# Kernel tuning notes

Hardware: AMD Instinct MI355X
Metric: run time of the kernel (lower is better)

Reference implementation:

```python
import jax, jax.numpy as jnp
import numpy as np

B, T, C, H = 2, 2048, 1024, 16
R = 32
LORA_SCALE = 0.5  # lora_alpha / r = (0.5*rank) / rank
HD = C // H


def setup_inputs() -> dict:
    key = jax.random.key(0)
    ks = jax.random.split(key, 8)
    std = 0.02
    return {
        "x": jax.random.normal(ks[0], (B, T, C), jnp.float32),
        "w_attn": jax.random.normal(ks[1], (3 * C, C), jnp.float32) * std,
        "b_attn": jnp.zeros((3 * C,), jnp.float32),
        "la_attn": jax.random.normal(ks[2], (R, C), jnp.float32) * std,
        "lb_attn": jax.random.normal(ks[3], (3 * C, R), jnp.float32) * std,
        "w_proj": jax.random.normal(ks[4], (C, C), jnp.float32) * std,
        "b_proj": jnp.zeros((C,), jnp.float32),
        "la_proj": jax.random.normal(ks[5], (R, C), jnp.float32) * std,
        "lb_proj": jax.random.normal(ks[6], (C, R), jnp.float32) * std,
    }


def lora_linear(x, w, b, la, lb):
    # y = x @ W^T + b + scale * (x @ A^T) @ B^T
    return x @ w.T + b + LORA_SCALE * ((x @ la.T) @ lb.T)


def reference(x, w_attn, b_attn, la_attn, lb_attn, w_proj, b_proj, la_proj, lb_proj):
    Bsz, Tlen, Cdim = x.shape
    qkv = lora_linear(x, w_attn, b_attn, la_attn, lb_attn)  # [B,T,3C]
    q, k, v = jnp.split(qkv, 3, axis=2)
    # [B,T,C] -> [B,H,T,hd]
    rs = lambda t: t.reshape(Bsz, Tlen, H, HD).transpose(0, 2, 1, 3)
    q, k, v = rs(q), rs(k), rs(v)
    att = jnp.einsum("bhqd,bhkd->bhqk", q, k) * (1.0 / np.sqrt(HD))
    causal = jnp.tril(jnp.ones((Tlen, Tlen), dtype=bool))
    att = jnp.where(causal[None, None], att, -jnp.inf)
    att = jax.nn.softmax(att, axis=-1)
    y = jnp.einsum("bhqk,bhkd->bhqd", att, v)  # [B,H,T,hd]
    y = y.transpose(0, 2, 1, 3).reshape(Bsz, Tlen, Cdim)
    return lora_linear(y, w_proj, b_proj, la_proj, lb_proj)
```

## Files before the change

kernel.cpp:

```cpp
#include <hip/hip_runtime.h>
#include <hip/hip_bf16.h>


typedef __attribute__((ext_vector_type(8))) short short8;
typedef __attribute__((ext_vector_type(4))) float float4v;

#define QSCALE 0.18033688011112292f

static __device__ __forceinline__ float b2f(ushort u) {
  union { uint i; float f; } v; v.i = ((uint)u) << 16; return v.f;
}
static __device__ __forceinline__ ushort f2b(float f) {
  union { float f; uint i; } v; v.f = f;
  uint i = v.i + 0x7fffu + ((v.i >> 16) & 1u);
  return (ushort)(i >> 16);
}
static __device__ __forceinline__ float4v zero4() {
  float4v z = {0.f, 0.f, 0.f, 0.f}; return z;
}
static __device__ __forceinline__ void glld16(const void* g, void* l) {
  __builtin_amdgcn_global_load_lds((const __attribute__((address_space(1))) void*)g,
                                   (__attribute__((address_space(3))) void*)l,
                                   16, 0, 0);
}

__global__ __launch_bounds__(256) void convert_all(
    const float* __restrict__ x, const float* __restrict__ wa,
    const float* __restrict__ la, const float* __restrict__ lb,
    const float* __restrict__ wp, const float* __restrict__ lp,
    const float* __restrict__ lq,
    ushort* __restrict__ xb, ushort* __restrict__ wab, ushort* __restrict__ lab,
    ushort* __restrict__ lbb, ushort* __restrict__ wpb, ushort* __restrict__ lpb,
    ushort* __restrict__ lqb) {
  const int stride = gridDim.x * blockDim.x;
  for (int i = blockIdx.x * blockDim.x + threadIdx.x; i < 2146304; i += stride) {
    const float* s; ushort* d; int off;
    if (i < 1048576)      { s = x;  d = xb;  off = i; }
    else if (i < 1835008) { s = wa; d = wab; off = i - 1048576; }
    else if (i < 1843200) { s = la; d = lab; off = i - 1835008; }
    else if (i < 1867776) { s = lb; d = lbb; off = i - 1843200; }
    else if (i < 2129920) { s = wp; d = wpb; off = i - 1867776; }
    else if (i < 2138112) { s = lp; d = lpb; off = i - 2129920; }
    else                  { s = lq; d = lqb; off = i - 2138112; }
    float4 v = ((const float4*)s)[off];
    union { ushort u[4]; uint2 p; } o;
    o.u[0] = f2b(v.x); o.u[1] = f2b(v.y); o.u[2] = f2b(v.z); o.u[3] = f2b(v.w);
    ((uint2*)d)[off] = o.p;
  }
}

__global__ __launch_bounds__(256) void lora_t(
    const ushort* __restrict__ X, const ushort* __restrict__ La,
    ushort* __restrict__ T) {
  const int tid = threadIdx.x;
  const int m = blockIdx.x * 8 + (tid >> 5);
  const int r = tid & 31;
  const uint4* xr = (const uint4*)(X + (size_t)m * 1024);
  const uint4* lr = (const uint4*)(La + (size_t)r * 1024);
  float s = 0.f;
#pragma unroll 4
  for (int kk = 0; kk < 128; ++kk) {
    uint4 xv = xr[kk], lv = lr[kk];
    s += b2f((ushort)xv.x) * b2f((ushort)lv.x) + b2f((ushort)(xv.x >> 16)) * b2f((ushort)(lv.x >> 16));
    s += b2f((ushort)xv.y) * b2f((ushort)lv.y) + b2f((ushort)(xv.y >> 16)) * b2f((ushort)(lv.y >> 16));
    s += b2f((ushort)xv.z) * b2f((ushort)lv.z) + b2f((ushort)(xv.z >> 16)) * b2f((ushort)(lv.z >> 16));
    s += b2f((ushort)xv.w) * b2f((ushort)lv.w) + b2f((ushort)(xv.w >> 16)) * b2f((ushort)(lv.w >> 16));
  }
  T[(size_t)m * 32 + r] = f2b(0.5f * s);
}

template <bool OUTF32, bool VSPLIT, int NBX>
__global__ __launch_bounds__(256) void gemm_lora(
    const ushort* __restrict__ A, const ushort* __restrict__ W,
    const float* __restrict__ bias,
    const ushort* __restrict__ T1, const ushort* __restrict__ Lb,
    void* __restrict__ outv, ushort* __restrict__ vt, int K, int ldo) {
  __shared__ __attribute__((aligned(16))) ushort As[2][128 * 32];
  __shared__ __attribute__((aligned(16))) ushort Ws[2][128 * 32];
  const int tid = threadIdx.x;
  const int lane = tid & 63, wv = tid >> 6;
  const int l15 = lane & 15, quad = lane >> 4;
  const int L = blockIdx.x;
  const int x8 = L & 7, q = L >> 3;
  const int bx = q % NBX;
  const int by = x8 * 4 + q / NBX;
  const int m0 = by * 128, n0 = bx * 128;
  const int wm = (wv >> 1) * 64, wn = (wv & 1) * 64;
  const int r4 = lane >> 2, c4 = (lane & 3) * 8;
  const int KT = K >> 5;

  float4v acc[4][4];
#pragma unroll
  for (int i = 0; i < 4; i++)
#pragma unroll
    for (int j = 0; j < 4; j++) acc[i][j] = zero4();

  auto stage = [&](int t, int buf) {
    const ushort* sA; const ushort* sW; int ld, k0;
    if (t < KT) { sA = A; sW = W; ld = K; k0 = t * 32; }
    else        { sA = T1; sW = Lb; ld = 32; k0 = 0; }
#pragma unroll
    for (int u = 0; u < 2; ++u) {
      int R = wv * 32 + u * 16;
      glld16(sA + (size_t)(m0 + R + r4) * ld + k0 + c4, &As[buf][R * 32]);
      glld16(sW + (size_t)(n0 + R + r4) * ld + k0 + c4, &Ws[buf][R * 32]);
    }
  };

  stage(0, 0);
  for (int t = 0; t <= KT; ++t) {
    __syncthreads();
    if (t < KT) stage(t + 1, (t + 1) & 1);
    const int b = t & 1;
    short8 af[4], wf[4];
#pragma unroll
    for (int i = 0; i < 4; i++)
      af[i] = *(const short8*)&As[b][(wm + i * 16 + l15) * 32 + quad * 8];
#pragma unroll
    for (int j = 0; j < 4; j++)
      wf[j] = *(const short8*)&Ws[b][(wn + j * 16 + l15) * 32 + quad * 8];
#pragma unroll
    for (int i = 0; i < 4; i++)
#pragma unroll
      for (int j = 0; j < 4; j++)
        acc[i][j] = __builtin_amdgcn_mfma_f32_16x16x32_bf16(af[i], wf[j], acc[i][j], 0, 0, 0);
  }

  const float qsc = (VSPLIT && n0 < 1024) ? QSCALE : 1.0f;
#pragma unroll
  for (int i = 0; i < 4; i++) {
    int gm = m0 + wm + i * 16 + quad * 4;
#pragma unroll
    for (int j = 0; j < 4; j++) {
      int gn = n0 + wn + j * 16 + l15;
      float bb = bias[gn];
      if (VSPLIT && n0 >= 2048) {
        int vc = gn - 2048;
        int bb2 = gm >> 11, t = gm & 2047;
        ushort u0 = f2b(acc[i][j][0] + bb), u1 = f2b(acc[i][j][1] + bb);
        ushort u2 = f2b(acc[i][j][2] + bb), u3 = f2b(acc[i][j][3] + bb);
        uint2 pk; pk.x = (uint)u0 | ((uint)u1 << 16); pk.y = (uint)u2 | ((uint)u3 << 16);
        *(uint2*)(vt + ((size_t)bb2 * 1024 + vc) * 2048 + t) = pk;
      } else {
#pragma unroll
        for (int r = 0; r < 4; r++) {
          float val = (acc[i][j][r] + bb) * qsc;
          if (OUTF32) ((float*)outv)[(size_t)(gm + r) * ldo + gn] = val;
          else        ((ushort*)outv)[(size_t)(gm + r) * ldo + gn] = f2b(val);
        }
      }
    }
  }
}

__global__ __launch_bounds__(256) void flash_attn(
    const ushort* __restrict__ qk, const ushort* __restrict__ vt,
    ushort* __restrict__ y) {
  __shared__ __attribute__((aligned(16))) ushort Ks[2][64 * 64];
  __shared__ __attribute__((aligned(16))) ushort Vts[2][64 * 64];
  __shared__ __attribute__((aligned(16))) ushort Ps[4 * 32 * 68];
  const int tid = threadIdx.x;
  const int lane = tid & 63, wv = tid >> 6;
  const int l15 = lane & 15, quad = lane >> 4;
  const int bid = blockIdx.x;
  const int idx = bid & 255;
  const int bh = idx & 31;
  const int g = idx >> 5;
  const int qb = (bid < 256) ? (15 - g) : g;
  const int b = bh >> 4, h = bh & 15;
  const ushort* qbase = qk + (size_t)b * 2048 * 2048 + h * 64;
  const ushort* kbase = qk + (size_t)b * 2048 * 2048 + 1024 + h * 64;
  const ushort* vbase = vt + ((size_t)b * 1024 + h * 64) * 2048;
  const int r8 = lane >> 3, c8 = (lane & 7) * 8;
  const int rotc = (c8 + r8 * 8) & 63;
  const int colk0 = (quad * 8 + 64 - 8 * (l15 & 7)) & 63;
  const int colk1 = (colk0 + 32) & 63;

#pragma unroll
  for (int u = 0; u < 4; ++u) {
    int R = wv * 32 + u * 8;
    glld16(qbase + (size_t)(qb * 128 + R + r8) * 2048 + rotc, &Ps[R * 64]);
  }
#pragma unroll
  for (int u = 0; u < 2; ++u) {
    int R = wv * 16 + u * 8;
    glld16(kbase + (size_t)(R + r8) * 2048 + rotc, &Ks[0][R * 64]);
    glld16(vbase + (size_t)(R + r8) * 2048 + rotc, &Vts[0][R * 64]);
  }
  __syncthreads();
  short8 aq[2][2];
#pragma unroll
  for (int i = 0; i < 2; ++i) {
    const int w = wv * 32 + i * 16 + l15;
    aq[i][0] = *(const short8*)&Ps[w * 64 + colk0];
    aq[i][1] = *(const short8*)&Ps[w * 64 + colk1];
  }
  __syncthreads();

  short8 ones;
#pragma unroll
  for (int e = 0; e < 8; e++) ones[e] = (short)0x3F80;

  float4v acc[2][4];
  float4v lacc[2];
#pragma unroll
  for (int i = 0; i < 2; ++i) {
    lacc[i] = zero4();
#pragma unroll
    for (int jt = 0; jt < 4; jt++) acc[i][jt] = zero4();
  }
  const int last = 2 * qb + 1;
  const int pB = wv * 32 * 68;

  for (int kb = 0; kb <= last; ++kb) {
    const int cur = kb & 1;
    if (kb < last) {
      const int nb = cur ^ 1;
#pragma unroll
      for (int u = 0; u < 2; ++u) {
        int R = wv * 16 + u * 8;
        glld16(kbase + (size_t)((kb + 1) * 64 + R + r8) * 2048 + rotc, &Ks[nb][R * 64]);
        glld16(vbase + (size_t)(R + r8) * 2048 + (kb + 1) * 64 + rotc, &Vts[nb][R * 64]);
      }
    }
    float4v s[2][4];
#pragma unroll
    for (int i = 0; i < 2; ++i)
#pragma unroll
      for (int j = 0; j < 4; ++j) s[i][j] = zero4();
#pragma unroll
    for (int j = 0; j < 4; ++j) {
      short8 bk0 = *(const short8*)&Ks[cur][(j * 16 + l15) * 64 + colk0];
      short8 bk1 = *(const short8*)&Ks[cur][(j * 16 + l15) * 64 + colk1];
#pragma unroll
      for (int i = 0; i < 2; ++i) {
        s[i][j] = __builtin_amdgcn_mfma_f32_16x16x32_bf16(aq[i][0], bk0, s[i][j], 0, 0, 0);
        s[i][j] = __builtin_amdgcn_mfma_f32_16x16x32_bf16(aq[i][1], bk1, s[i][j], 0, 0, 0);
      }
    }
#pragma unroll
    for (int i = 0; i < 2; ++i) {
      const int qrow_i = qb * 128 + wv * 32 + i * 16;
      if (kb * 64 + 63 > qrow_i) {
#pragma unroll
        for (int j = 0; j < 4; ++j) {
          int key = kb * 64 + j * 16 + l15;
#pragma unroll
          for (int r = 0; r < 4; ++r)
            if (key > qrow_i + quad * 4 + r) s[i][j][r] = -1e30f;
        }
      }
    }
#pragma unroll
    for (int i = 0; i < 2; ++i)
#pragma unroll
      for (int j = 0; j < 4; ++j)
#pragma unroll
        for (int r = 0; r < 4; ++r) {
          float pv = exp2f(s[i][j][r]);
          union { float f; uint u; } cv; cv.f = pv;
          Ps[pB + (i * 16 + quad * 4 + r) * 68 + j * 16 + l15] = (ushort)(cv.u >> 16);
        }
#pragma unroll
    for (int kt2 = 0; kt2 < 2; ++kt2) {
      const int vcol = kt2 ? colk1 : colk0;
      short8 pa[2];
#pragma unroll
      for (int i = 0; i < 2; ++i) {
        pa[i] = *(const short8*)&Ps[pB + (i * 16 + l15) * 68 + kt2 * 32 + quad * 8];
        lacc[i] = __builtin_amdgcn_mfma_f32_16x16x32_bf16(pa[i], ones, lacc[i], 0, 0, 0);
      }
#pragma unroll
      for (int jt = 0; jt < 4; ++jt) {
        short8 vb = *(const short8*)&Vts[cur][(jt * 16 + l15) * 64 + vcol];
#pragma unroll
        for (int i = 0; i < 2; ++i)
          acc[i][jt] = __builtin_amdgcn_mfma_f32_16x16x32_bf16(pa[i], vb, acc[i][jt], 0, 0, 0);
      }
    }
    __syncthreads();
  }
#pragma unroll
  for (int i = 0; i < 2; ++i)
#pragma unroll
    for (int r = 0; r < 4; ++r) {
      float inv = __builtin_amdgcn_rcpf(lacc[i][r]);
      int t = qb * 128 + wv * 32 + i * 16 + quad * 4 + r;
#pragma unroll
      for (int jt = 0; jt < 4; ++jt)
        y[(size_t)(b * 2048 + t) * 1024 + h * 64 + jt * 16 + l15] =
            f2b(acc[i][jt][r] * inv);
    }
}

extern "C" void kernel_launch(void* const* d_in, const int* in_sizes, int n_in,
                              void* d_out, int out_size, void* d_ws, size_t ws_size,
                              hipStream_t stream) {
  const float* x       = (const float*)d_in[0];
  const float* w_attn  = (const float*)d_in[1];
  const float* b_attn  = (const float*)d_in[2];
  const float* la_attn = (const float*)d_in[3];
  const float* lb_attn = (const float*)d_in[4];
  const float* w_proj  = (const float*)d_in[5];
  const float* b_proj  = (const float*)d_in[6];
  const float* la_proj = (const float*)d_in[7];
  const float* lb_proj = (const float*)d_in[8];

  ushort* p = (ushort*)d_ws;
  ushort* xb   = p; p += (size_t)4096 * 1024;
  ushort* wab  = p; p += (size_t)3072 * 1024;
  ushort* lab  = p; p += (size_t)32 * 1024;
  ushort* lbb  = p; p += (size_t)3072 * 32;
  ushort* wpb  = p; p += (size_t)1024 * 1024;
  ushort* lpb  = p; p += (size_t)32 * 1024;
  ushort* lqb  = p; p += (size_t)1024 * 32;
  ushort* t1b  = p; p += (size_t)4096 * 32;
  ushort* t2b  = p; p += (size_t)4096 * 32;
  ushort* qkb  = p; p += (size_t)4096 * 2048;
  ushort* vtb  = p; p += (size_t)2048 * 2048;
  ushort* yb   = p; p += (size_t)4096 * 1024;

  convert_all<<<dim3(2048), dim3(256), 0, stream>>>(
      x, w_attn, la_attn, lb_attn, w_proj, la_proj, lb_proj,
      xb, wab, lab, lbb, wpb, lpb, lqb);
  lora_t<<<dim3(512), dim3(256), 0, stream>>>(xb, lab, t1b);
  gemm_lora<false, true, 24><<<dim3(768), dim3(256), 0, stream>>>(
      xb, wab, b_attn, t1b, lbb, qkb, vtb, 1024, 2048);
  flash_attn<<<dim3(512), dim3(256), 0, stream>>>(qkb, vtb, yb);
  lora_t<<<dim3(512), dim3(256), 0, stream>>>(yb, lpb, t2b);
  gemm_lora<true, false, 8><<<dim3(256), dim3(256), 0, stream>>>(
      yb, wpb, b_proj, t2b, lqb, d_out, nullptr, 1024, 1024);
}
```

Baseline: 282.2 us.

## Pair heavy and light causal query tiles in one 512-thread flash-attention block

The flash-attention kernel now launches 256 blocks of 512 threads. Each block handles a high query tile (waves 0-3) and its mirrored low query tile (waves 4-7) for the same batch-head. The two tiles share every K/V tile loaded into LDS, which halves K/V global traffic and evens out causal work per block. The P buffer gets an XOR-style column swizzle in place of row padding, and the head-to-block mapping is permuted. The cost is that the low-tile waves sit idle at barriers after their last block, and occupancy per CU changes with the larger block.

```diff
diff --git a/kernel.cpp b/kernel.cpp
--- a/kernel.cpp
+++ b/kernel.cpp
@@ -153,49 +153,50 @@
   }
 }
 
-__global__ __launch_bounds__(256) void flash_attn(
+__global__ __launch_bounds__(512) void flash_attn(
     const ushort* __restrict__ qk, const ushort* __restrict__ vt,
     ushort* __restrict__ y) {
   __shared__ __attribute__((aligned(16))) ushort Ks[2][64 * 64];
   __shared__ __attribute__((aligned(16))) ushort Vts[2][64 * 64];
-  __shared__ __attribute__((aligned(16))) ushort Ps[4 * 32 * 68];
+  __shared__ __attribute__((aligned(16))) ushort Ps[8 * 32 * 64];
   const int tid = threadIdx.x;
   const int lane = tid & 63, wv = tid >> 6;
   const int l15 = lane & 15, quad = lane >> 4;
-  const int bid = blockIdx.x;
-  const int idx = bid & 255;
-  const int bh = idx & 31;
-  const int g = idx >> 5;
-  const int qb = (bid < 256) ? (15 - g) : g;
+  const int L = blockIdx.x;
+  const int bh = (L & 7) * 4 + ((L >> 3) & 3);
+  const int g = L >> 5;
   const int b = bh >> 4, h = bh & 15;
+  const int qbH = 15 - g, qbL = g;
+  const int qtile = (wv < 4) ? qbH : qbL;
+  const int wl = wv & 3;
+  const int lastH = 2 * qbH + 1;
+  const int lastL = 2 * qbL + 1;
   const ushort* qbase = qk + (size_t)b * 2048 * 2048 + h * 64;
   const ushort* kbase = qk + (size_t)b * 2048 * 2048 + 1024 + h * 64;
   const ushort* vbase = vt + ((size_t)b * 1024 + h * 64) * 2048;
   const int r8 = lane >> 3, c8 = (lane & 7) * 8;
-  const int rotc = (c8 + r8 * 8) & 63;
+  const int rotKV = (c8 + 8 * r8) & 63;
   const int colk0 = (quad * 8 + 64 - 8 * (l15 & 7)) & 63;
   const int colk1 = (colk0 + 32) & 63;
-
+  const int pcol0 = (quad * 8 + 64 - 8 * (l15 >> 1)) & 63;
+  const int pcol1 = (pcol0 + 32) & 63;
+  const int pB = wv * 2048;
+
+  const int qr0 = qtile * 128 + wl * 32;
 #pragma unroll
   for (int u = 0; u < 4; ++u) {
-    int R = wv * 32 + u * 8;
-    glld16(qbase + (size_t)(qb * 128 + R + r8) * 2048 + rotc, &Ps[R * 64]);
-  }
-#pragma unroll
-  for (int u = 0; u < 2; ++u) {
-    int R = wv * 16 + u * 8;
-    glld16(kbase + (size_t)(R + r8) * 2048 + rotc, &Ks[0][R * 64]);
-    glld16(vbase + (size_t)(R + r8) * 2048 + rotc, &Vts[0][R * 64]);
-  }
+    int rotQ = (c8 + 8 * ((u * 4 + (r8 >> 1)) & 7)) & 63;
+    glld16(qbase + (size_t)(qr0 + u * 8 + r8) * 2048 + rotQ, &Ps[pB + u * 8 * 64]);
+  }
+  glld16(kbase + (size_t)(wv * 8 + r8) * 2048 + rotKV, &Ks[0][wv * 8 * 64]);
+  glld16(vbase + (size_t)(wv * 8 + r8) * 2048 + rotKV, &Vts[0][wv * 8 * 64]);
   __syncthreads();
   short8 aq[2][2];
 #pragma unroll
   for (int i = 0; i < 2; ++i) {
-    const int w = wv * 32 + i * 16 + l15;
-    aq[i][0] = *(const short8*)&Ps[w * 64 + colk0];
-    aq[i][1] = *(const short8*)&Ps[w * 64 + colk1];
-  }
-  __syncthreads();
+    aq[i][0] = *(const short8*)&Ps[pB + (i * 16 + l15) * 64 + pcol0];
+    aq[i][1] = *(const short8*)&Ps[pB + (i * 16 + l15) * 64 + pcol1];
+  }
 
   short8 ones;
 #pragma unroll
@@ -209,73 +210,73 @@
 #pragma unroll
     for (int jt = 0; jt < 4; jt++) acc[i][jt] = zero4();
   }
-  const int last = 2 * qb + 1;
-  const int pB = wv * 32 * 68;
-
-  for (int kb = 0; kb <= last; ++kb) {
+
+  for (int kb = 0; kb <= lastH; ++kb) {
     const int cur = kb & 1;
-    if (kb < last) {
+    if (kb < lastH) {
       const int nb = cur ^ 1;
-#pragma unroll
-      for (int u = 0; u < 2; ++u) {
-        int R = wv * 16 + u * 8;
-        glld16(kbase + (size_t)((kb + 1) * 64 + R + r8) * 2048 + rotc, &Ks[nb][R * 64]);
-        glld16(vbase + (size_t)(R + r8) * 2048 + (kb + 1) * 64 + rotc, &Vts[nb][R * 64]);
+      glld16(kbase + (size_t)((kb + 1) * 64 + wv * 8 + r8) * 2048 + rotKV,
+             &Ks[nb][wv * 8 * 64]);
+      glld16(vbase + (size_t)(wv * 8 + r8) * 2048 + (kb + 1) * 64 + rotKV,
+             &Vts[nb][wv * 8 * 64]);
+    }
+    if (wv < 4 || kb <= lastL) {
+      float4v s[2][4];
+#pragma unroll
+      for (int i = 0; i < 2; ++i)
+#pragma unroll
+        for (int j = 0; j < 4; ++j) s[i][j] = zero4();
+#pragma unroll
+      for (int j = 0; j < 4; ++j) {
+        short8 bk0 = *(const short8*)&Ks[cur][(j * 16 + l15) * 64 + colk0];
+        short8 bk1 = *(const short8*)&Ks[cur][(j * 16 + l15) * 64 + colk1];
+#pragma unroll
+        for (int i = 0; i < 2; ++i) {
+          s[i][j] = __builtin_amdgcn_mfma_f32_16x16x32_bf16(aq[i][0], bk0, s[i][j], 0, 0, 0);
+          s[i][j] = __builtin_amdgcn_mfma_f32_16x16x32_bf16(aq[i][1], bk1, s[i][j], 0, 0, 0);
+        }
       }
-    }
-    float4v s[2][4];
-#pragma unroll
-    for (int i = 0; i < 2; ++i)
-#pragma unroll
-      for (int j = 0; j < 4; ++j) s[i][j] = zero4();
-#pragma unroll
-    for (int j = 0; j < 4; ++j) {
-      short8 bk0 = *(const short8*)&Ks[cur][(j * 16 + l15) * 64 + colk0];
-      short8 bk1 = *(const short8*)&Ks[cur][(j * 16 + l15) * 64 + colk1];
 #pragma unroll
       for (int i = 0; i < 2; ++i) {
-        s[i][j] = __builtin_amdgcn_mfma_f32_16x16x32_bf16(aq[i][0], bk0, s[i][j], 0, 0, 0);
-        s[i][j] = __builtin_amdgcn_mfma_f32_16x16x32_bf16(aq[i][1], bk1, s[i][j], 0, 0, 0);
+        const int qrow_i = qtile * 128 + wl * 32 + i * 16;
+        if (kb * 64 + 63 > qrow_i) {
+#pragma unroll
+          for (int j = 0; j < 4; ++j) {
+            int key = kb * 64 + j * 16 + l15;
+#pragma unroll
+            for (int r = 0; r < 4; ++r)
+              if (key > qrow_i + quad * 4 + r) s[i][j][r] = -1e30f;
+          }
+        }
       }
-    }
-#pragma unroll
-    for (int i = 0; i < 2; ++i) {
-      const int qrow_i = qb * 128 + wv * 32 + i * 16;
-      if (kb * 64 + 63 > qrow_i) {
-#pragma unroll
-        for (int j = 0; j < 4; ++j) {
-          int key = kb * 64 + j * 16 + l15;
-#pragma unroll
-          for (int r = 0; r < 4; ++r)
-            if (key > qrow_i + quad * 4 + r) s[i][j][r] = -1e30f;
-        }
-      }
-    }
-#pragma unroll
-    for (int i = 0; i < 2; ++i)
-#pragma unroll
-      for (int j = 0; j < 4; ++j)
-#pragma unroll
-        for (int r = 0; r < 4; ++r) {
-          float pv = exp2f(s[i][j][r]);
-          union { float f; uint u; } cv; cv.f = pv;
-          Ps[pB + (i * 16 + quad * 4 + r) * 68 + j * 16 + l15] = (ushort)(cv.u >> 16);
-        }
-#pragma unroll
-    for (int kt2 = 0; kt2 < 2; ++kt2) {
-      const int vcol = kt2 ? colk1 : colk0;
-      short8 pa[2];
-#pragma unroll
-      for (int i = 0; i < 2; ++i) {
-        pa[i] = *(const short8*)&Ps[pB + (i * 16 + l15) * 68 + kt2 * 32 + quad * 8];
-        lacc[i] = __builtin_amdgcn_mfma_f32_16x16x32_bf16(pa[i], ones, lacc[i], 0, 0, 0);
-      }
-#pragma unroll
-      for (int jt = 0; jt < 4; ++jt) {
-        short8 vb = *(const short8*)&Vts[cur][(jt * 16 + l15) * 64 + vcol];
-#pragma unroll
-        for (int i = 0; i < 2; ++i)
-          acc[i][jt] = __builtin_amdgcn_mfma_f32_16x16x32_bf16(pa[i], vb, acc[i][jt], 0, 0, 0);
+#pragma unroll
+      for (int i = 0; i < 2; ++i)
+#pragma unroll
+        for (int j = 0; j < 4; ++j)
+#pragma unroll
+          for (int r = 0; r < 4; ++r) {
+            float pv = exp2f(s[i][j][r]);
+            union { float f; uint u; } cv; cv.f = pv;
+            int wcol = (j * 16 + l15 + 64 - 8 * ((quad * 2 + (r >> 1)) & 7)) & 63;
+            Ps[pB + (i * 16 + quad * 4 + r) * 64 + wcol] = (ushort)(cv.u >> 16);
+          }
+#pragma unroll
+      for (int kt2 = 0; kt2 < 2; ++kt2) {
+        const int vcol = kt2 ? colk1 : colk0;
+        const int pcol = kt2 ? pcol1 : pcol0;
+        short8 pa[2];
+#pragma unroll
+        for (int i = 0; i < 2; ++i) {
+          pa[i] = *(const short8*)&Ps[pB + (i * 16 + l15) * 64 + pcol];
+          lacc[i] = __builtin_amdgcn_mfma_f32_16x16x32_bf16(pa[i], ones, lacc[i], 0, 0, 0);
+        }
+#pragma unroll
+        for (int jt = 0; jt < 4; ++jt) {
+          short8 vb = *(const short8*)&Vts[cur][(jt * 16 + l15) * 64 + vcol];
+#pragma unroll
+          for (int i = 0; i < 2; ++i)
+            acc[i][jt] = __builtin_amdgcn_mfma_f32_16x16x32_bf16(pa[i], vb, acc[i][jt], 0, 0, 0);
+        }
       }
     }
     __syncthreads();
@@ -285,7 +286,7 @@
 #pragma unroll
     for (int r = 0; r < 4; ++r) {
       float inv = __builtin_amdgcn_rcpf(lacc[i][r]);
-      int t = qb * 128 + wv * 32 + i * 16 + quad * 4 + r;
+      int t = qtile * 128 + wl * 32 + i * 16 + quad * 4 + r;
 #pragma unroll
       for (int jt = 0; jt < 4; ++jt)
         y[(size_t)(b * 2048 + t) * 1024 + h * 64 + jt * 16 + l15] =
@@ -326,7 +327,7 @@
   lora_t<<<dim3(512), dim3(256), 0, stream>>>(xb, lab, t1b);
   gemm_lora<false, true, 24><<<dim3(768), dim3(256), 0, stream>>>(
       xb, wab, b_attn, t1b, lbb, qkb, vtb, 1024, 2048);
-  flash_attn<<<dim3(512), dim3(256), 0, stream>>>(qkb, vtb, yb);
+  flash_attn<<<dim3(256), dim3(512), 0, stream>>>(qkb, vtb, yb);
   lora_t<<<dim3(512), dim3(256), 0, stream>>>(yb, lpb, t2b);
   gemm_lora<true, false, 8><<<dim3(256), dim3(256), 0, stream>>>(
       yb, wpb, b_proj, t2b, lqb, d_out, nullptr, 1024, 1024);
```

After: 273.4 us. 1.03x faster.

## Pair high and low causal query tiles per block with 64-row waves

Applied to the files above, without the earlier changes.

Each attention block now processes two query tiles (a late one and an early one) with the same head, waves 0-1 handling the high tile and waves 2-3 the low tile. Each wave owns 64 query rows, so the grid halves and the shared K/V stream is loaded once for both tiles, balancing the causal work inside a block. S is computed transposed (K as the A operand) so P can be written to LDS as packed 4-element stores in a rotated layout, and the extra sync after the Q load is removed. The cost is more accumulator registers per wave (16 acc tiles), idle low-tile waves once they pass their last key block, and fewer blocks to fill the GPU.

```diff
diff --git a/kernel.cpp b/kernel.cpp
--- a/kernel.cpp
+++ b/kernel.cpp
@@ -158,29 +158,35 @@
     ushort* __restrict__ y) {
   __shared__ __attribute__((aligned(16))) ushort Ks[2][64 * 64];
   __shared__ __attribute__((aligned(16))) ushort Vts[2][64 * 64];
-  __shared__ __attribute__((aligned(16))) ushort Ps[4 * 32 * 68];
+  __shared__ __attribute__((aligned(16))) ushort Ps[4 * 64 * 64];
   const int tid = threadIdx.x;
   const int lane = tid & 63, wv = tid >> 6;
   const int l15 = lane & 15, quad = lane >> 4;
-  const int bid = blockIdx.x;
-  const int idx = bid & 255;
-  const int bh = idx & 31;
-  const int g = idx >> 5;
-  const int qb = (bid < 256) ? (15 - g) : g;
+  const int L = blockIdx.x;
+  const int bh = (L & 7) * 4 + ((L >> 3) & 3);
+  const int g = L >> 5;
   const int b = bh >> 4, h = bh & 15;
+  const int qbH = 15 - g, qbL = g;
+  const int qtile = (wv < 2) ? qbH : qbL;
+  const int qrow0 = qtile * 128 + (wv & 1) * 64;
+  const int myLast = 2 * qtile + (wv & 1);
+  const int lastH = 2 * qbH + 1;
   const ushort* qbase = qk + (size_t)b * 2048 * 2048 + h * 64;
   const ushort* kbase = qk + (size_t)b * 2048 * 2048 + 1024 + h * 64;
   const ushort* vbase = vt + ((size_t)b * 1024 + h * 64) * 2048;
   const int r8 = lane >> 3, c8 = (lane & 7) * 8;
-  const int rotc = (c8 + r8 * 8) & 63;
-  const int colk0 = (quad * 8 + 64 - 8 * (l15 & 7)) & 63;
+  const int rotc = (c8 + 8 * r8) & 63;
+  const int m8 = l15 & 7;
+  const int colk0 = (quad * 8 + 64 - 8 * m8) & 63;
   const int colk1 = (colk0 + 32) & 63;
-
-#pragma unroll
-  for (int u = 0; u < 4; ++u) {
-    int R = wv * 32 + u * 8;
-    glld16(qbase + (size_t)(qb * 128 + R + r8) * 2048 + rotc, &Ps[R * 64]);
-  }
+  int wcol[4];
+#pragma unroll
+  for (int jk = 0; jk < 4; ++jk) wcol[jk] = (jk * 16 + quad * 4 + 64 - 8 * m8) & 63;
+  const int pB = wv * 4096;
+
+#pragma unroll
+  for (int u = 0; u < 8; ++u)
+    glld16(qbase + (size_t)(qrow0 + u * 8 + r8) * 2048 + rotc, &Ps[pB + u * 8 * 64]);
 #pragma unroll
   for (int u = 0; u < 2; ++u) {
     int R = wv * 16 + u * 8;
@@ -188,33 +194,29 @@
     glld16(vbase + (size_t)(R + r8) * 2048 + rotc, &Vts[0][R * 64]);
   }
   __syncthreads();
-  short8 aq[2][2];
-#pragma unroll
-  for (int i = 0; i < 2; ++i) {
-    const int w = wv * 32 + i * 16 + l15;
-    aq[i][0] = *(const short8*)&Ps[w * 64 + colk0];
-    aq[i][1] = *(const short8*)&Ps[w * 64 + colk1];
-  }
-  __syncthreads();
+  short8 aq[4][2];
+#pragma unroll
+  for (int iq = 0; iq < 4; ++iq) {
+    aq[iq][0] = *(const short8*)&Ps[pB + (iq * 16 + l15) * 64 + colk0];
+    aq[iq][1] = *(const short8*)&Ps[pB + (iq * 16 + l15) * 64 + colk1];
+  }
 
   short8 ones;
 #pragma unroll
   for (int e = 0; e < 8; e++) ones[e] = (short)0x3F80;
 
-  float4v acc[2][4];
-  float4v lacc[2];
-#pragma unroll
-  for (int i = 0; i < 2; ++i) {
+  float4v acc[4][4];
+  float4v lacc[4];
+#pragma unroll
+  for (int i = 0; i < 4; ++i) {
     lacc[i] = zero4();
 #pragma unroll
     for (int jt = 0; jt < 4; jt++) acc[i][jt] = zero4();
   }
-  const int last = 2 * qb + 1;
-  const int pB = wv * 32 * 68;
-
-  for (int kb = 0; kb <= last; ++kb) {
+
+  for (int kb = 0; kb <= lastH; ++kb) {
     const int cur = kb & 1;
-    if (kb < last) {
+    if (kb < lastH) {
       const int nb = cur ^ 1;
 #pragma unroll
       for (int u = 0; u < 2; ++u) {
@@ -223,73 +225,68 @@
         glld16(vbase + (size_t)(R + r8) * 2048 + (kb + 1) * 64 + rotc, &Vts[nb][R * 64]);
       }
     }
-    float4v s[2][4];
-#pragma unroll
-    for (int i = 0; i < 2; ++i)
-#pragma unroll
-      for (int j = 0; j < 4; ++j) s[i][j] = zero4();
-#pragma unroll
-    for (int j = 0; j < 4; ++j) {
-      short8 bk0 = *(const short8*)&Ks[cur][(j * 16 + l15) * 64 + colk0];
-      short8 bk1 = *(const short8*)&Ks[cur][(j * 16 + l15) * 64 + colk1];
-#pragma unroll
-      for (int i = 0; i < 2; ++i) {
-        s[i][j] = __builtin_amdgcn_mfma_f32_16x16x32_bf16(aq[i][0], bk0, s[i][j], 0, 0, 0);
-        s[i][j] = __builtin_amdgcn_mfma_f32_16x16x32_bf16(aq[i][1], bk1, s[i][j], 0, 0, 0);
+    if (kb <= myLast) {
+#pragma unroll
+      for (int jk = 0; jk < 4; ++jk) {
+        short8 bk0 = *(const short8*)&Ks[cur][(jk * 16 + l15) * 64 + colk0];
+        short8 bk1 = *(const short8*)&Ks[cur][(jk * 16 + l15) * 64 + colk1];
+        float4v s[4];
+#pragma unroll
+        for (int iq = 0; iq < 4; ++iq) {
+          s[iq] = __builtin_amdgcn_mfma_f32_16x16x32_bf16(bk0, aq[iq][0], zero4(), 0, 0, 0);
+          s[iq] = __builtin_amdgcn_mfma_f32_16x16x32_bf16(bk1, aq[iq][1], s[iq], 0, 0, 0);
+        }
+        if (kb == myLast) {
+          const int key0 = kb * 64 + jk * 16 + quad * 4;
+#pragma unroll
+          for (int iq = 0; iq < 4; ++iq) {
+            const int qg = qrow0 + iq * 16 + l15;
+#pragma unroll
+            for (int r = 0; r < 4; ++r)
+              if (key0 + r > qg) s[iq][r] = -1e30f;
+          }
+        }
+#pragma unroll
+        for (int iq = 0; iq < 4; ++iq) {
+          union { float f; uint u; } c0, c1, c2, c3;
+          c0.f = exp2f(s[iq][0]); c1.f = exp2f(s[iq][1]);
+          c2.f = exp2f(s[iq][2]); c3.f = exp2f(s[iq][3]);
+          uint2 pk;
+          pk.x = (c0.u >> 16) | (c1.u & 0xffff0000u);
+          pk.y = (c2.u >> 16) | (c3.u & 0xffff0000u);
+          *(uint2*)&Ps[pB + (iq * 16 + l15) * 64 + wcol[jk]] = pk;
+        }
       }
-    }
-#pragma unroll
-    for (int i = 0; i < 2; ++i) {
-      const int qrow_i = qb * 128 + wv * 32 + i * 16;
-      if (kb * 64 + 63 > qrow_i) {
-#pragma unroll
-        for (int j = 0; j < 4; ++j) {
-          int key = kb * 64 + j * 16 + l15;
-#pragma unroll
-          for (int r = 0; r < 4; ++r)
-            if (key > qrow_i + quad * 4 + r) s[i][j][r] = -1e30f;
+#pragma unroll
+      for (int kt2 = 0; kt2 < 2; ++kt2) {
+        const int vcol = kt2 ? colk1 : colk0;
+        short8 pa[4];
+#pragma unroll
+        for (int iq = 0; iq < 4; ++iq) {
+          pa[iq] = *(const short8*)&Ps[pB + (iq * 16 + l15) * 64 + vcol];
+          lacc[iq] = __builtin_amdgcn_mfma_f32_16x16x32_bf16(pa[iq], ones, lacc[iq], 0, 0, 0);
+        }
+#pragma unroll
+        for (int jt = 0; jt < 4; ++jt) {
+          short8 vb = *(const short8*)&Vts[cur][(jt * 16 + l15) * 64 + vcol];
+#pragma unroll
+          for (int iq = 0; iq < 4; ++iq)
+            acc[iq][jt] = __builtin_amdgcn_mfma_f32_16x16x32_bf16(pa[iq], vb, acc[iq][jt], 0, 0, 0);
         }
       }
     }
-#pragma unroll
-    for (int i = 0; i < 2; ++i)
-#pragma unroll
-      for (int j = 0; j < 4; ++j)
-#pragma unroll
-        for (int r = 0; r < 4; ++r) {
-          float pv = exp2f(s[i][j][r]);
-          union { float f; uint u; } cv; cv.f = pv;
-          Ps[pB + (i * 16 + quad * 4 + r) * 68 + j * 16 + l15] = (ushort)(cv.u >> 16);
-        }
-#pragma unroll
-    for (int kt2 = 0; kt2 < 2; ++kt2) {
-      const int vcol = kt2 ? colk1 : colk0;
-      short8 pa[2];
-#pragma unroll
-      for (int i = 0; i < 2; ++i) {
-        pa[i] = *(const short8*)&Ps[pB + (i * 16 + l15) * 68 + kt2 * 32 + quad * 8];
-        lacc[i] = __builtin_amdgcn_mfma_f32_16x16x32_bf16(pa[i], ones, lacc[i], 0, 0, 0);
-      }
-#pragma unroll
-      for (int jt = 0; jt < 4; ++jt) {
-        short8 vb = *(const short8*)&Vts[cur][(jt * 16 + l15) * 64 + vcol];
-#pragma unroll
-        for (int i = 0; i < 2; ++i)
-          acc[i][jt] = __builtin_amdgcn_mfma_f32_16x16x32_bf16(pa[i], vb, acc[i][jt], 0, 0, 0);
-      }
-    }
     __syncthreads();
   }
 #pragma unroll
-  for (int i = 0; i < 2; ++i)
+  for (int iq = 0; iq < 4; ++iq)
 #pragma unroll
     for (int r = 0; r < 4; ++r) {
-      float inv = __builtin_amdgcn_rcpf(lacc[i][r]);
-      int t = qb * 128 + wv * 32 + i * 16 + quad * 4 + r;
+      float inv = __builtin_amdgcn_rcpf(lacc[iq][r]);
+      int t = qrow0 + iq * 16 + quad * 4 + r;
 #pragma unroll
       for (int jt = 0; jt < 4; ++jt)
         y[(size_t)(b * 2048 + t) * 1024 + h * 64 + jt * 16 + l15] =
-            f2b(acc[i][jt][r] * inv);
+            f2b(acc[iq][jt][r] * inv);
     }
 }
 
@@ -326,7 +323,7 @@
   lora_t<<<dim3(512), dim3(256), 0, stream>>>(xb, lab, t1b);
   gemm_lora<false, true, 24><<<dim3(768), dim3(256), 0, stream>>>(
       xb, wab, b_attn, t1b, lbb, qkb, vtb, 1024, 2048);
-  flash_attn<<<dim3(512), dim3(256), 0, stream>>>(qkb, vtb, yb);
+  flash_attn<<<dim3(256), dim3(256), 0, stream>>>(qkb, vtb, yb);
   lora_t<<<dim3(512), dim3(256), 0, stream>>>(yb, lpb, t2b);
   gemm_lora<true, false, 8><<<dim3(256), dim3(256), 0, stream>>>(
       yb, wpb, b_proj, t2b, lqb, d_out, nullptr, 1024, 1024);
```

After: 301.4 us. 6.8% more time.
